# Kernel tuning notes

Measured on AMD Instinct MI355X. Metric: run time of the kernel, lower is better.

Reference implementation:

```python
import jax, jax.numpy as jnp
import numpy as np

N_NODES = 100000
N_EDGES = 1600000
IN_F = 128
OUT_F = 64
ORDER = 3


def setup_inputs() -> dict:
    key = jax.random.key(0)
    k1, k2, k3, k4, k5 = jax.random.split(key, 5)
    x = jax.random.normal(k1, (N_NODES, IN_F), dtype=jnp.float32)
    edge_index = jax.random.randint(k2, (2, N_EDGES), 0, N_NODES, dtype=jnp.int64)
    edge_weight = jax.random.uniform(k3, (N_EDGES,), dtype=jnp.float32)
    # nn.Linear default init scale ~ 1/sqrt(in_features)
    W_weight = jax.random.normal(k4, (OUT_F, IN_F), dtype=jnp.float32) / np.sqrt(IN_F)
    W_bias = jax.random.normal(k5, (OUT_F,), dtype=jnp.float32) / np.sqrt(IN_F)
    return {"x": x, "edge_index": edge_index, "edge_weight": edge_weight,
            "W_weight": W_weight, "W_bias": W_bias}


def _spmm(edge_index, edge_weight, h):
    # out[dst] = sum_e edge_weight[e] * h[src[e]]
    src, dst = edge_index[0], edge_index[1]
    msg = edge_weight[:, None] * h[src]          # [E, OUT_F] gathered messages
    return jax.ops.segment_sum(msg, dst, num_segments=N_NODES)


def reference(x, edge_index, edge_weight, W_weight, W_bias):
    # Linear projection: [N, IN_F] -> [N, OUT_F]
    h = x @ W_weight.T + W_bias
    # `order` hops of sparse propagation
    for _ in range(ORDER):
        h = _spmm(edge_index, edge_weight, h)
    return h
```

## Files before the change

kernel.cpp:

```cpp
#include <hip/hip_runtime.h>
#include <hip/hip_fp16.h>

#define N_NODES_C 100000
#define N_EDGES_C 1600000
#define IN_F 128
#define OUT_F 64

#define BIN_SHIFT 9
#define BIN_SZ    512
#define NBIN      ((N_NODES_C + BIN_SZ - 1) / BIN_SZ)
#define NCHUNK    256
#define CH        (N_EDGES_C / NCHUNK)

typedef __attribute__((ext_vector_type(8))) _Float16 half8;
typedef __attribute__((ext_vector_type(4))) float    f32x4;

__global__ __launch_bounds__(256) void gemm_mfma_kernel(
    const float* __restrict__ x, const float* __restrict__ W,
    const float* __restrict__ bias, _Float16* __restrict__ h, int n) {
  const int wid  = threadIdx.x >> 6;
  const int lane = threadIdx.x & 63;
  const int lr   = lane & 15;
  const int lg   = lane >> 4;

  const int tile = blockIdx.x * 4 + wid;
  if (tile * 16 >= n) return;
  const int node0 = tile * 16;

  half8 bfrag[4][4];
#pragma unroll
  for (int nc = 0; nc < 4; ++nc) {
    const float* wrow = W + (size_t)(nc * 16 + lr) * IN_F + lg * 8;
#pragma unroll
    for (int kc = 0; kc < 4; ++kc) {
      float4 a = ((const float4*)(wrow + kc * 32))[0];
      float4 b = ((const float4*)(wrow + kc * 32))[1];
      half8 f;
      f[0] = (_Float16)a.x; f[1] = (_Float16)a.y;
      f[2] = (_Float16)a.z; f[3] = (_Float16)a.w;
      f[4] = (_Float16)b.x; f[5] = (_Float16)b.y;
      f[6] = (_Float16)b.z; f[7] = (_Float16)b.w;
      bfrag[nc][kc] = f;
    }
  }

  float bv[4];
#pragma unroll
  for (int nc = 0; nc < 4; ++nc) bv[nc] = bias[nc * 16 + lr];

  const float* xp = x + (size_t)(node0 + lr) * IN_F + lg * 8;
  f32x4 acc[4] = {{0.f, 0.f, 0.f, 0.f}, {0.f, 0.f, 0.f, 0.f},
                  {0.f, 0.f, 0.f, 0.f}, {0.f, 0.f, 0.f, 0.f}};
#pragma unroll
  for (int kc = 0; kc < 4; ++kc) {
    float4 a = ((const float4*)(xp + kc * 32))[0];
    float4 b = ((const float4*)(xp + kc * 32))[1];
    half8 af;
    af[0] = (_Float16)a.x; af[1] = (_Float16)a.y;
    af[2] = (_Float16)a.z; af[3] = (_Float16)a.w;
    af[4] = (_Float16)b.x; af[5] = (_Float16)b.y;
    af[6] = (_Float16)b.z; af[7] = (_Float16)b.w;
#pragma unroll
    for (int nc = 0; nc < 4; ++nc)
      acc[nc] = __builtin_amdgcn_mfma_f32_16x16x32_f16(af, bfrag[nc][kc], acc[nc], 0, 0, 0);
  }

#pragma unroll
  for (int nc = 0; nc < 4; ++nc) {
#pragma unroll
    for (int r = 0; r < 4; ++r) {
      int node = node0 + lg * 4 + r;
      h[(size_t)node * OUT_F + nc * 16 + lr] = (_Float16)(acc[nc][r] + bv[nc]);
    }
  }
}

__global__ __launch_bounds__(1024) void hist_kernel(
    const int* __restrict__ dst, int* __restrict__ hist) {
  __shared__ int h[NBIN];
  const int t = threadIdx.x;
  for (int i = t; i < NBIN; i += 1024) h[i] = 0;
  __syncthreads();
  const int e0 = blockIdx.x * CH;
  for (int i = t; i < CH; i += 1024)
    atomicAdd(&h[dst[e0 + i] >> BIN_SHIFT], 1);
  __syncthreads();
  for (int i = t; i < NBIN; i += 1024)
    hist[i * NCHUNK + blockIdx.x] = h[i];
}

__global__ __launch_bounds__(1024) void scan_all_kernel(
    const int* __restrict__ hist, int* __restrict__ soff,
    int* __restrict__ binStart) {
  __shared__ __align__(16) int binTot[256];
  __shared__ __align__(16) int binBase[256];
  const int t = threadIdx.x;
  const int w = t >> 6, lane = t & 63;

  for (int b = w; b < NBIN; b += 16) {
    int4 v = ((const int4*)(hist + (size_t)b * NCHUNK))[lane];
    int s = v.x + v.y + v.z + v.w;
#pragma unroll
    for (int off = 1; off < 64; off <<= 1) s += __shfl_xor(s, off);
    if (lane == 0) binTot[b] = s;
  }
  if (t >= NBIN && t < 256) binTot[t] = 0;
  __syncthreads();

  if (w == 0) {
    int4 v = ((const int4*)binTot)[lane];
    int s0 = v.x, s1 = s0 + v.y, s2 = s1 + v.z, s3 = s2 + v.w;
    int ls = s3;
#pragma unroll
    for (int off = 1; off < 64; off <<= 1) {
      int u = __shfl_up(ls, off);
      if (lane >= off) ls += u;
    }
    int ex = ls - s3;
    int4 o;
    o.x = ex; o.y = ex + s0; o.z = ex + s1; o.w = ex + s2;
    ((int4*)binBase)[lane] = o;
  }
  __syncthreads();

  if (t < NBIN) binStart[t] = binBase[t];

  for (int b = w; b < NBIN; b += 16) {
    int base = binBase[b];
    int4 v = ((const int4*)(hist + (size_t)b * NCHUNK))[lane];
    int s0 = v.x, s1 = s0 + v.y, s2 = s1 + v.z, s3 = s2 + v.w;
    int ls = s3;
#pragma unroll
    for (int off = 1; off < 64; off <<= 1) {
      int u = __shfl_up(ls, off);
      if (lane >= off) ls += u;
    }
    int ex = base + ls - s3;
    int4 o;
    o.x = ex; o.y = ex + s0; o.z = ex + s1; o.w = ex + s2;
    ((int4*)(soff + (size_t)b * NCHUNK))[lane] = o;
  }
}

__global__ __launch_bounds__(1024) void binscatter_kernel(
    const int* __restrict__ src, const int* __restrict__ dst,
    const float* __restrict__ w, const int* __restrict__ soff,
    int* __restrict__ stage_d, int2* __restrict__ stage_sw) {
  __shared__ int lcur[NBIN];
  const int t = threadIdx.x;
  const int c = blockIdx.x;
  for (int i = t; i < NBIN; i += 1024) lcur[i] = soff[i * NCHUNK + c];
  __syncthreads();
  const int e0 = c * CH;
  for (int i = t; i < CH; i += 1024) {
    int e = e0 + i;
    int d = dst[e];
    int p = atomicAdd(&lcur[d >> BIN_SHIFT], 1);
    stage_d[p]  = d;
    stage_sw[p] = make_int2(src[e] * OUT_F, __float_as_int(w[e]));
  }
}

__global__ __launch_bounds__(1024) void place_kernel(
    const int* __restrict__ binStart, const int* __restrict__ stage_d,
    const int2* __restrict__ stage_sw, int* __restrict__ row_ptr,
    int2* __restrict__ edges, int n) {
  __shared__ int lcount[BIN_SZ];
  __shared__ int s[BIN_SZ];
  __shared__ int lcur[BIN_SZ];
  const int t = threadIdx.x;
  const int b = blockIdx.x;
  const int base = binStart[b];
  const int end  = (b == NBIN - 1) ? N_EDGES_C : binStart[b + 1];
  const int node0 = b << BIN_SHIFT;

  if (t < BIN_SZ) lcount[t] = 0;
  __syncthreads();
  for (int i = base + t; i < end; i += 1024)
    atomicAdd(&lcount[stage_d[i] - node0], 1);
  __syncthreads();

  int v = 0;
  if (t < BIN_SZ) { v = lcount[t]; s[t] = v; }
  __syncthreads();
  for (int off = 1; off < BIN_SZ; off <<= 1) {
    int u = (t < BIN_SZ && t >= off) ? s[t - off] : 0;
    __syncthreads();
    if (t < BIN_SZ) s[t] += u;
    __syncthreads();
  }
  if (t < BIN_SZ) {
    int ex = base + s[t] - v;
    int node = node0 + t;
    if (node < n) row_ptr[node] = ex;
    lcur[t] = ex;
  }
  __syncthreads();

  for (int i = base + t; i < end; i += 1024) {
    int d = stage_d[i];
    int p = atomicAdd(&lcur[d - node0], 1);
    edges[p] = stage_sw[i];
  }
  if (b == NBIN - 1 && t == 0) row_ptr[n] = N_EDGES_C;
}

__device__ inline void fma8_h(float* acc, uint4 r, float w) {
  unsigned u[4] = {r.x, r.y, r.z, r.w};
#pragma unroll
  for (int q = 0; q < 4; ++q) {
    __half2 h2 = *reinterpret_cast<__half2*>(&u[q]);
    float2 f = __half22float2(h2);
    acc[2 * q + 0] += w * f.x;
    acc[2 * q + 1] += w * f.y;
  }
}

template <int OUT32>
__global__ __launch_bounds__(256) void spmm16_kernel(
    const int* __restrict__ row_ptr, const int2* __restrict__ edges,
    const __half* __restrict__ hin, void* __restrict__ hout, int n) {
  const int node = blockIdx.x * 32 + (threadIdx.x >> 3);
  const int fl   = threadIdx.x & 7;
  if (node >= n) return;
  const int beg = row_ptr[node];
  const int end = row_ptr[node + 1];

  float acc[8] = {0.f, 0.f, 0.f, 0.f, 0.f, 0.f, 0.f, 0.f};
  int j = beg;
  for (; j + 3 < end; j += 4) {
    int2 e0 = edges[j + 0];
    int2 e1 = edges[j + 1];
    int2 e2 = edges[j + 2];
    int2 e3 = edges[j + 3];
    uint4 r0 = ((const uint4*)(hin + e0.x))[fl];
    uint4 r1 = ((const uint4*)(hin + e1.x))[fl];
    uint4 r2 = ((const uint4*)(hin + e2.x))[fl];
    uint4 r3 = ((const uint4*)(hin + e3.x))[fl];
    fma8_h(acc, r0, __int_as_float(e0.y));
    fma8_h(acc, r1, __int_as_float(e1.y));
    fma8_h(acc, r2, __int_as_float(e2.y));
    fma8_h(acc, r3, __int_as_float(e3.y));
  }
  for (; j < end; ++j) {
    int2 e = edges[j];
    uint4 r = ((const uint4*)(hin + e.x))[fl];
    fma8_h(acc, r, __int_as_float(e.y));
  }

  if (OUT32) {
    float* op = (float*)hout + (size_t)node * OUT_F + 8 * fl;
    ((float4*)op)[0] = make_float4(acc[0], acc[1], acc[2], acc[3]);
    ((float4*)op)[1] = make_float4(acc[4], acc[5], acc[6], acc[7]);
  } else {
    union { __half2 h2[4]; uint4 u; } pk;
#pragma unroll
    for (int q = 0; q < 4; ++q)
      pk.h2[q] = __floats2half2_rn(acc[2 * q], acc[2 * q + 1]);
    ((uint4*)((char*)hout + (size_t)node * 128))[fl] = pk.u;
  }
}

extern "C" void kernel_launch(void* const* d_in, const int* in_sizes, int n_in,
                              void* d_out, int out_size, void* d_ws, size_t ws_size,
                              hipStream_t stream) {
  const float* x    = (const float*)d_in[0];
  const int*   ei   = (const int*)d_in[1];
  const float* ew   = (const float*)d_in[2];
  const float* W    = (const float*)d_in[3];
  const float* bias = (const float*)d_in[4];
  float* out = (float*)d_out;

  const int N = N_NODES_C;
  const int E = N_EDGES_C;
  const int* src = ei;
  const int* dst = ei + E;
  const int NH = NBIN * NCHUNK;

  char* p = (char*)d_ws;
  auto carve = [&](size_t bytes) {
    void* r = (void*)p;
    p += (bytes + 255) & ~(size_t)255;
    return r;
  };
  __half* h16A     = (__half*)carve((size_t)N * OUT_F * 2);
  __half* h16B     = (__half*)carve((size_t)N * OUT_F * 2);
  int*   row_ptr   = (int*)  carve((size_t)(N + 1) * 4);
  int2*  edges     = (int2*) carve((size_t)E * 8);
  int*   hist      = (int*)  carve((size_t)NH * 4);
  int*   soff      = (int*)  carve((size_t)NH * 4);
  int*   binStart  = (int*)  carve((size_t)(NBIN + 1) * 4);

  int2* stage_sw = (int2*)d_out;
  int*  stage_d  = (int*)((char*)d_out + (size_t)E * 8);

  gemm_mfma_kernel<<<(N / 16 + 3) / 4, 256, 0, stream>>>(x, W, bias, (_Float16*)h16A, N);
  hist_kernel      <<<NCHUNK, 1024, 0, stream>>>(dst, hist);
  scan_all_kernel  <<<1, 1024, 0, stream>>>(hist, soff, binStart);
  binscatter_kernel<<<NCHUNK, 1024, 0, stream>>>(src, dst, ew, soff, stage_d, stage_sw);
  place_kernel     <<<NBIN, 1024, 0, stream>>>(binStart, stage_d, stage_sw,
                                               row_ptr, edges, N);
  spmm16_kernel<0><<<(N + 31) / 32, 256, 0, stream>>>(row_ptr, edges, h16A, h16B, N);
  spmm16_kernel<0><<<(N + 31) / 32, 256, 0, stream>>>(row_ptr, edges, h16B, h16A, N);
  spmm16_kernel<1><<<(N + 31) / 32, 256, 0, stream>>>(row_ptr, edges, h16A, out, N);
}
```

Before: 289.3 us.

## Fuse CSR build stages into one cooperative kernel with grid syncs

Replaces the four CSR-construction kernels (histogram, scan, bin scatter, place) with a single cooperative-launch kernel using grid.sync between phases. The scan is split into a parallel per-bin reduction, a single-block exclusive scan, and a parallel per-bin prefix pass. The intent is to remove kernel launch gaps and the serial single-block scan. It adds grid-wide barriers, larger shared-memory use per block, and it depends on all 256 blocks of 1024 threads being co-resident.

```diff
diff --git a/kernel.cpp b/kernel.cpp
--- a/kernel.cpp
+++ b/kernel.cpp
@@ -1,5 +1,8 @@
 #include <hip/hip_runtime.h>
 #include <hip/hip_fp16.h>
+#include <hip/hip_cooperative_groups.h>
+
+namespace cg = cooperative_groups;
 
 #define N_NODES_C 100000
 #define N_EDGES_C 1600000
@@ -75,134 +78,132 @@
   }
 }
 
-__global__ __launch_bounds__(1024) void hist_kernel(
-    const int* __restrict__ dst, int* __restrict__ hist) {
-  __shared__ int h[NBIN];
-  const int t = threadIdx.x;
-  for (int i = t; i < NBIN; i += 1024) h[i] = 0;
-  __syncthreads();
-  const int e0 = blockIdx.x * CH;
-  for (int i = t; i < CH; i += 1024)
-    atomicAdd(&h[dst[e0 + i] >> BIN_SHIFT], 1);
-  __syncthreads();
-  for (int i = t; i < NBIN; i += 1024)
-    hist[i * NCHUNK + blockIdx.x] = h[i];
-}
-
-__global__ __launch_bounds__(1024) void scan_all_kernel(
-    const int* __restrict__ hist, int* __restrict__ soff,
-    int* __restrict__ binStart) {
-  __shared__ __align__(16) int binTot[256];
-  __shared__ __align__(16) int binBase[256];
-  const int t = threadIdx.x;
-  const int w = t >> 6, lane = t & 63;
-
-  for (int b = w; b < NBIN; b += 16) {
-    int4 v = ((const int4*)(hist + (size_t)b * NCHUNK))[lane];
-    int s = v.x + v.y + v.z + v.w;
-#pragma unroll
-    for (int off = 1; off < 64; off <<= 1) s += __shfl_xor(s, off);
-    if (lane == 0) binTot[b] = s;
-  }
-  if (t >= NBIN && t < 256) binTot[t] = 0;
-  __syncthreads();
-
-  if (w == 0) {
-    int4 v = ((const int4*)binTot)[lane];
-    int s0 = v.x, s1 = s0 + v.y, s2 = s1 + v.z, s3 = s2 + v.w;
-    int ls = s3;
+__global__ __launch_bounds__(1024) void mega_csr_kernel(
+    const int* __restrict__ src, const int* __restrict__ dst,
+    const float* __restrict__ ew, int* __restrict__ hist,
+    int* __restrict__ rowTot, int* __restrict__ binStart,
+    int* __restrict__ soff, int* __restrict__ stage_d,
+    int2* __restrict__ stage_sw, int* __restrict__ row_ptr,
+    int2* __restrict__ edges, int n) {
+  cg::grid_group grid = cg::this_grid();
+  const int t   = threadIdx.x;
+  const int bid = blockIdx.x;
+
+  __shared__ int hh[NBIN];
+  __shared__ int red[16];
+  __shared__ int s3[256];
+  __shared__ int wsum[16];
+  __shared__ int lcur[NBIN];
+  __shared__ int lcount[BIN_SZ];
+  __shared__ int s6[BIN_SZ];
+  __shared__ int lcur6[BIN_SZ];
+
+  if (bid < NCHUNK) {
+    for (int i = t; i < NBIN; i += 1024) hh[i] = 0;
+    __syncthreads();
+    const int e0 = bid * CH;
+    for (int i = t; i < CH; i += 1024)
+      atomicAdd(&hh[dst[e0 + i] >> BIN_SHIFT], 1);
+    __syncthreads();
+    for (int i = t; i < NBIN; i += 1024)
+      hist[i * NCHUNK + bid] = hh[i];
+  }
+  grid.sync();
+
+  if (bid < NBIN) {
+    int v = (t < NCHUNK) ? hist[bid * NCHUNK + t] : 0;
+#pragma unroll
+    for (int off = 1; off < 64; off <<= 1) v += __shfl_xor(v, off);
+    if ((t & 63) == 0) red[t >> 6] = v;
+    __syncthreads();
+    if (t == 0) rowTot[bid] = red[0] + red[1] + red[2] + red[3];
+  }
+  grid.sync();
+
+  if (bid == 0) {
+    int v = (t < NBIN) ? rowTot[t] : 0;
+    if (t < 256) s3[t] = v;
+    __syncthreads();
+    for (int off = 1; off < 256; off <<= 1) {
+      int u = 0;
+      if (t < 256 && t >= off) u = s3[t - off];
+      __syncthreads();
+      if (t < 256) s3[t] += u;
+      __syncthreads();
+    }
+    if (t < NBIN) binStart[t] = s3[t] - v;
+  }
+  grid.sync();
+
+  if (bid < NBIN) {
+    int base = binStart[bid];
+    int v = (t < NCHUNK) ? hist[bid * NCHUNK + t] : 0;
+    int ls = v;
 #pragma unroll
     for (int off = 1; off < 64; off <<= 1) {
       int u = __shfl_up(ls, off);
-      if (lane >= off) ls += u;
-    }
-    int ex = ls - s3;
-    int4 o;
-    o.x = ex; o.y = ex + s0; o.z = ex + s1; o.w = ex + s2;
-    ((int4*)binBase)[lane] = o;
-  }
-  __syncthreads();
-
-  if (t < NBIN) binStart[t] = binBase[t];
-
-  for (int b = w; b < NBIN; b += 16) {
-    int base = binBase[b];
-    int4 v = ((const int4*)(hist + (size_t)b * NCHUNK))[lane];
-    int s0 = v.x, s1 = s0 + v.y, s2 = s1 + v.z, s3 = s2 + v.w;
-    int ls = s3;
-#pragma unroll
-    for (int off = 1; off < 64; off <<= 1) {
-      int u = __shfl_up(ls, off);
-      if (lane >= off) ls += u;
-    }
-    int ex = base + ls - s3;
-    int4 o;
-    o.x = ex; o.y = ex + s0; o.z = ex + s1; o.w = ex + s2;
-    ((int4*)(soff + (size_t)b * NCHUNK))[lane] = o;
-  }
-}
-
-__global__ __launch_bounds__(1024) void binscatter_kernel(
-    const int* __restrict__ src, const int* __restrict__ dst,
-    const float* __restrict__ w, const int* __restrict__ soff,
-    int* __restrict__ stage_d, int2* __restrict__ stage_sw) {
-  __shared__ int lcur[NBIN];
-  const int t = threadIdx.x;
-  const int c = blockIdx.x;
-  for (int i = t; i < NBIN; i += 1024) lcur[i] = soff[i * NCHUNK + c];
-  __syncthreads();
-  const int e0 = c * CH;
-  for (int i = t; i < CH; i += 1024) {
-    int e = e0 + i;
-    int d = dst[e];
-    int p = atomicAdd(&lcur[d >> BIN_SHIFT], 1);
-    stage_d[p]  = d;
-    stage_sw[p] = make_int2(src[e] * OUT_F, __float_as_int(w[e]));
-  }
-}
-
-__global__ __launch_bounds__(1024) void place_kernel(
-    const int* __restrict__ binStart, const int* __restrict__ stage_d,
-    const int2* __restrict__ stage_sw, int* __restrict__ row_ptr,
-    int2* __restrict__ edges, int n) {
-  __shared__ int lcount[BIN_SZ];
-  __shared__ int s[BIN_SZ];
-  __shared__ int lcur[BIN_SZ];
-  const int t = threadIdx.x;
-  const int b = blockIdx.x;
-  const int base = binStart[b];
-  const int end  = (b == NBIN - 1) ? N_EDGES_C : binStart[b + 1];
-  const int node0 = b << BIN_SHIFT;
-
-  if (t < BIN_SZ) lcount[t] = 0;
-  __syncthreads();
-  for (int i = base + t; i < end; i += 1024)
-    atomicAdd(&lcount[stage_d[i] - node0], 1);
-  __syncthreads();
-
-  int v = 0;
-  if (t < BIN_SZ) { v = lcount[t]; s[t] = v; }
-  __syncthreads();
-  for (int off = 1; off < BIN_SZ; off <<= 1) {
-    int u = (t < BIN_SZ && t >= off) ? s[t - off] : 0;
-    __syncthreads();
-    if (t < BIN_SZ) s[t] += u;
-    __syncthreads();
-  }
-  if (t < BIN_SZ) {
-    int ex = base + s[t] - v;
-    int node = node0 + t;
-    if (node < n) row_ptr[node] = ex;
-    lcur[t] = ex;
-  }
-  __syncthreads();
-
-  for (int i = base + t; i < end; i += 1024) {
-    int d = stage_d[i];
-    int p = atomicAdd(&lcur[d - node0], 1);
-    edges[p] = stage_sw[i];
-  }
-  if (b == NBIN - 1 && t == 0) row_ptr[n] = N_EDGES_C;
+      if ((t & 63) >= off) ls += u;
+    }
+    if ((t & 63) == 63) wsum[t >> 6] = ls;
+    __syncthreads();
+    int wv = t >> 6;
+    int woff = 0;
+    if (wv >= 1) woff = wsum[0];
+    if (wv >= 2) woff += wsum[1];
+    if (wv >= 3) woff += wsum[2];
+    if (t < NCHUNK) soff[bid * NCHUNK + t] = base + woff + ls - v;
+  }
+  grid.sync();
+
+  if (bid < NCHUNK) {
+    for (int i = t; i < NBIN; i += 1024) lcur[i] = soff[i * NCHUNK + bid];
+    __syncthreads();
+    const int e0 = bid * CH;
+    for (int i = t; i < CH; i += 1024) {
+      int e = e0 + i;
+      int d = dst[e];
+      int p = atomicAdd(&lcur[d >> BIN_SHIFT], 1);
+      stage_d[p]  = d;
+      stage_sw[p] = make_int2(src[e] * OUT_F, __float_as_int(ew[e]));
+    }
+  }
+  grid.sync();
+
+  if (bid < NBIN) {
+    const int base = binStart[bid];
+    const int end  = (bid == NBIN - 1) ? N_EDGES_C : binStart[bid + 1];
+    const int node0 = bid << BIN_SHIFT;
+
+    if (t < BIN_SZ) lcount[t] = 0;
+    __syncthreads();
+    for (int i = base + t; i < end; i += 1024)
+      atomicAdd(&lcount[stage_d[i] - node0], 1);
+    __syncthreads();
+
+    int v = 0;
+    if (t < BIN_SZ) { v = lcount[t]; s6[t] = v; }
+    __syncthreads();
+    for (int off = 1; off < BIN_SZ; off <<= 1) {
+      int u = (t < BIN_SZ && t >= off) ? s6[t - off] : 0;
+      __syncthreads();
+      if (t < BIN_SZ) s6[t] += u;
+      __syncthreads();
+    }
+    if (t < BIN_SZ) {
+      int ex = base + s6[t] - v;
+      int node = node0 + t;
+      if (node < n) row_ptr[node] = ex;
+      lcur6[t] = ex;
+    }
+    __syncthreads();
+
+    for (int i = base + t; i < end; i += 1024) {
+      int d = stage_d[i];
+      int p = atomicAdd(&lcur6[d - node0], 1);
+      edges[p] = stage_sw[i];
+    }
+    if (bid == NBIN - 1 && t == 0) row_ptr[n] = N_EDGES_C;
+  }
 }
 
 __device__ inline void fma8_h(float* acc, uint4 r, float w) {
@@ -289,17 +290,24 @@
   int2*  edges     = (int2*) carve((size_t)E * 8);
   int*   hist      = (int*)  carve((size_t)NH * 4);
   int*   soff      = (int*)  carve((size_t)NH * 4);
+  int*   rowTot    = (int*)  carve((size_t)NBIN * 4);
   int*   binStart  = (int*)  carve((size_t)(NBIN + 1) * 4);
 
   int2* stage_sw = (int2*)d_out;
   int*  stage_d  = (int*)((char*)d_out + (size_t)E * 8);
 
+  {
+    int Nv = N;
+    void* margs[] = {(void*)&src, (void*)&dst, (void*)&ew, (void*)&hist,
+                     (void*)&rowTot, (void*)&binStart, (void*)&soff,
+                     (void*)&stage_d, (void*)&stage_sw, (void*)&row_ptr,
+                     (void*)&edges, (void*)&Nv};
+    hipLaunchCooperativeKernel((void*)mega_csr_kernel, dim3(NCHUNK), dim3(1024),
+                               margs, 0, stream);
+  }
+
   gemm_mfma_kernel<<<(N / 16 + 3) / 4, 256, 0, stream>>>(x, W, bias, (_Float16*)h16A, N);
-  hist_kernel      <<<NCHUNK, 1024, 0, stream>>>(dst, hist);
-  scan_all_kernel  <<<1, 1024, 0, stream>>>(hist, soff, binStart);
-  binscatter_kernel<<<NCHUNK, 1024, 0, stream>>>(src, dst, ew, soff, stage_d, stage_sw);
-  place_kernel     <<<NBIN, 1024, 0, stream>>>(binStart, stage_d, stage_sw,
-                                               row_ptr, edges, N);
+
   spmm16_kernel<0><<<(N + 31) / 32, 256, 0, stream>>>(row_ptr, edges, h16A, h16B, N);
   spmm16_kernel<0><<<(N + 31) / 32, 256, 0, stream>>>(row_ptr, edges, h16B, h16A, N);
   spmm16_kernel<1><<<(N + 31) / 32, 256, 0, stream>>>(row_ptr, edges, h16A, out, N);
```

After: 437.9 us. 51.4% more time.
